# Kernel tuning notes

Hardware: AMD Instinct MI355X
Metric: run time of the kernel (lower is better)

## Reference

```python
import jax, jax.numpy as jnp
import numpy as np

B, N, D, H = 4, 2048, 256, 8
DH = D // H

def setup_inputs() -> dict:
    key = jax.random.key(0)
    ks = jax.random.split(key, 7)
    s = 1.0 / np.sqrt(DH)
    return {
        "sequences": jax.random.normal(ks[0], (B, N, D), dtype=jnp.float32),
        "Wq": jax.random.uniform(ks[1], (H, DH, DH), jnp.float32, -s, s),
        "bq": jax.random.uniform(ks[2], (H, DH), jnp.float32, -s, s),
        "Wk": jax.random.uniform(ks[3], (H, DH, DH), jnp.float32, -s, s),
        "bk": jax.random.uniform(ks[4], (H, DH), jnp.float32, -s, s),
        "Wv": jax.random.uniform(ks[5], (H, DH, DH), jnp.float32, -s, s),
        "bv": jax.random.uniform(ks[6], (H, DH), jnp.float32, -s, s),
    }

def reference(sequences, Wq, bq, Wk, bk, Wv, bv):
    # sequences: [B, N, D] -> [B, N, H, DH] (head h sees columns h*DH:(h+1)*DH)
    x = sequences.reshape(B, N, H, DH)
    # per-head Linear: y = x @ W.T + b
    q = jnp.einsum("bnhd,hed->bnhe", x, Wq) + bq
    k = jnp.einsum("bnhd,hed->bnhe", x, Wk) + bk
    v = jnp.einsum("bnhd,hed->bnhe", x, Wv) + bv
    scores = jnp.einsum("bnhe,bmhe->bhnm", q, k) / jnp.sqrt(jnp.float32(DH))
    attn = jax.nn.softmax(scores, axis=-1)  # [B, H, N, N]
    out = jnp.einsum("bhnm,bmhe->bnhe", attn, v)
    # hstack of per-head results == concat over last dim == reshape
    return out.reshape(B, N, D)
```

## Files before the change

### kernel.cpp

```cpp
#include <hip/hip_runtime.h>
#include <hip/hip_bf16.h>

typedef __bf16 bf16;
typedef __bf16 bf16x8 __attribute__((ext_vector_type(8)));
typedef __bf16 bf16x4 __attribute__((ext_vector_type(4)));
typedef float  f32x4  __attribute__((ext_vector_type(4)));

#define B_  4
#define N_  2048
#define D_  256
#define H_  8
#define DH_ 32
#define QKV_ELEMS (B_*H_*N_*DH_)

#define QSC    (0.17677669529663687f * 1.4426950408889634f)
#define NBIAS  (-17.312340490667562f)

#if __has_builtin(__builtin_amdgcn_exp2f)
__device__ inline float exp2_hw(float x) { return __builtin_amdgcn_exp2f(x); }
#else
__device__ inline float exp2_hw(float x) {
    float r; asm volatile("v_exp_f32 %0, %1" : "=v"(r) : "v"(x)); return r;
}
#endif

__device__ inline void gload_lds16(const bf16* g, bf16* l) {
    __builtin_amdgcn_global_load_lds(
        (const __attribute__((address_space(1))) void*)g,
        (__attribute__((address_space(3))) void*)l, 16, 0, 0);
}

__device__ inline bf16x8 ldcvt8(const float* __restrict__ p) {
    f32x4 a = *(const f32x4*)p;
    f32x4 b = *(const f32x4*)(p + 4);
    bf16x8 r;
    r[0] = (bf16)a[0]; r[1] = (bf16)a[1]; r[2] = (bf16)a[2]; r[3] = (bf16)a[3];
    r[4] = (bf16)b[0]; r[5] = (bf16)b[1]; r[6] = (bf16)b[2]; r[7] = (bf16)b[3];
    return r;
}

__global__ __launch_bounds__(256, 4) void qkv_proj_kernel(
    const float* __restrict__ x,
    const float* __restrict__ Wq, const float* __restrict__ bq,
    const float* __restrict__ Wk, const float* __restrict__ bk,
    const float* __restrict__ Wv, const float* __restrict__ bv,
    bf16* __restrict__ Qg, bf16* __restrict__ Kg, bf16* __restrict__ Vg)
{
    const int bh = blockIdx.x & 31, nt = blockIdx.x >> 5;
    const int h  = bh & (H_-1),    b  = bh >> 3;
    const int wave = threadIdx.x >> 6, lane = threadIdx.x & 63;
    const int l16 = lane & 15, q4 = lane >> 4;
    const int n0 = nt*64 + wave*16;

    bf16x8 wqf[2], wkf[2], wvf[2];
    f32x4  bq4[2], bk4[2];
    float  bvs[2];
    #pragma unroll
    for (int half = 0; half < 2; ++half) {
        wqf[half] = ldcvt8(Wq + (h*DH_ + half*16 + l16)*DH_ + q4*8);
        wkf[half] = ldcvt8(Wk + (h*DH_ + half*16 + l16)*DH_ + q4*8);
        wvf[half] = ldcvt8(Wv + (h*DH_ + half*16 + l16)*DH_ + q4*8);
        bq4[half] = *(const f32x4*)(bq + h*DH_ + half*16 + q4*4);
        bk4[half] = *(const f32x4*)(bk + h*DH_ + half*16 + q4*4);
        bvs[half] = bv[h*DH_ + half*16 + l16];
    }

    bf16x8 xf = ldcvt8(x + ((size_t)(b*N_ + n0 + l16))*D_ + h*DH_ + q4*8);
    const f32x4 z = {0.f,0.f,0.f,0.f};

    #pragma unroll
    for (int half = 0; half < 2; ++half) {
        f32x4 dq = __builtin_amdgcn_mfma_f32_16x16x32_bf16(wqf[half], xf, z, 0, 0, 0);
        f32x4 dk = __builtin_amdgcn_mfma_f32_16x16x32_bf16(wkf[half], xf, z, 0, 0, 0);
        f32x4 dv = __builtin_amdgcn_mfma_f32_16x16x32_bf16(xf, wvf[half], z, 0, 0, 0);
        bf16x4 pq, pk, pv;
        #pragma unroll
        for (int r = 0; r < 4; ++r) {
            pq[r] = (bf16)((dq[r] + bq4[half][r]) * QSC);
            pk[r] = (bf16)(dk[r] + bk4[half][r]);
            pv[r] = (bf16)(dv[r] + bvs[half]);
        }
        const size_t row = ((size_t)bh*N_ + n0 + l16)*DH_ + half*16 + q4*4;
        *(bf16x4*)(Qg + row) = pq;
        *(bf16x4*)(Kg + row) = pk;
        const int e = half*16 + l16;
        const size_t idx = ((size_t)bh << 16) + ((size_t)(n0 >> 5) << 10)
                         + (e << 5) + (q4 << 3) + (((n0 >> 4) & 1) << 2);
        *(bf16x4*)(Vg + idx) = pv;
    }
}

__global__ __launch_bounds__(256, 2) void attn_kernel(
    const bf16* __restrict__ Qg, const bf16* __restrict__ Kg,
    const bf16* __restrict__ Vg, float* __restrict__ out)
{
    const int bh = blockIdx.x & 31;
    const int qt = blockIdx.x >> 5;
    const int h  = bh & (H_-1), b = bh >> 3;
    const int lane = threadIdx.x & 63;
    const int wave = threadIdx.x >> 6;
    const int l16 = lane & 15, q4 = lane >> 4;

    __shared__ bf16 Kl[4][128*DH_];
    __shared__ bf16 Vl[4][128*DH_];

    const bf16* Kb = Kg + (size_t)bh*N_*DH_;
    const bf16* Vb = Vg + ((size_t)bh << 16);
    const int qrow0 = qt*128 + wave*32;
    const int kt0 = ((qt*5 + bh) & 7)*2;

    bf16x8 qb0 = *(const bf16x8*)(Qg + ((size_t)bh*N_ + qrow0 + l16)*DH_ + q4*8);
    bf16x8 qb1 = *(const bf16x8*)(Qg + ((size_t)bh*N_ + qrow0 + 16 + l16)*DH_ + q4*8);

    bf16x8 ones;
    #pragma unroll
    for (int j = 0; j < 8; ++j) ones[j] = (bf16)1.0f;

    f32x4 ot[2][2];
    ot[0][0] = (f32x4){0,0,0,0}; ot[0][1] = (f32x4){0,0,0,0};
    ot[1][0] = (f32x4){0,0,0,0}; ot[1][1] = (f32x4){0,0,0,0};
    f32x4 osum0 = {0,0,0,0}, osum1 = {0,0,0,0};
    const f32x4 zb = {NBIAS, NBIAS, NBIAS, NBIAS};

    const int seg = wave*1024 + lane*8;

    #pragma unroll
    for (int d = 0; d < 2; ++d) {
        const int t = (kt0 + d) & 15;
        const bf16* gk = Kb + (size_t)t*4096 + seg;
        const bf16* gv = Vb + (size_t)t*4096 + seg;
        gload_lds16(gk,       &Kl[d][wave*1024]);
        gload_lds16(gk + 512, &Kl[d][wave*1024 + 512]);
        gload_lds16(gv,       &Vl[d][wave*1024]);
        gload_lds16(gv + 512, &Vl[d][wave*1024 + 512]);
    }
    __syncthreads();

    for (int p = 0; p < 8; ++p) {
        #pragma unroll
        for (int d = 2; d < 4; ++d) {
            const int t  = (kt0 + 2*p + d) & 15;
            const int bf = (2*p + d) & 3;
            const bf16* gk = Kb + (size_t)t*4096 + seg;
            const bf16* gv = Vb + (size_t)t*4096 + seg;
            gload_lds16(gk,       &Kl[bf][wave*1024]);
            gload_lds16(gk + 512, &Kl[bf][wave*1024 + 512]);
            gload_lds16(gv,       &Vl[bf][wave*1024]);
            gload_lds16(gv + 512, &Vl[bf][wave*1024 + 512]);
        }

        #pragma unroll
        for (int d = 0; d < 2; ++d) {
            const int bf = (2*p + d) & 3;
            f32x4 st[8][2];
            #pragma unroll
            for (int kc = 0; kc < 8; ++kc) {
                bf16x8 kf = *(const bf16x8*)(&Kl[bf][(kc*16 + l16)*DH_ + q4*8]);
                st[kc][0] = __builtin_amdgcn_mfma_f32_16x16x32_bf16(kf, qb0, zb, 0, 0, 0);
                st[kc][1] = __builtin_amdgcn_mfma_f32_16x16x32_bf16(kf, qb1, zb, 0, 0, 0);
            }
            #pragma unroll
            for (int kk = 0; kk < 4; ++kk) {
                bf16x8 pb0, pb1;
                #pragma unroll
                for (int hf = 0; hf < 2; ++hf)
                    #pragma unroll
                    for (int r = 0; r < 4; ++r) {
                        pb0[hf*4 + r] = (bf16)exp2_hw(st[kk*2 + hf][0][r]);
                        pb1[hf*4 + r] = (bf16)exp2_hw(st[kk*2 + hf][1][r]);
                    }
                bf16x8 v0 = *(const bf16x8*)(&Vl[bf][kk*1024 + l16*DH_ + q4*8]);
                bf16x8 v1 = *(const bf16x8*)(&Vl[bf][kk*1024 + (16 + l16)*DH_ + q4*8]);
                ot[0][0] = __builtin_amdgcn_mfma_f32_16x16x32_bf16(v0, pb0, ot[0][0], 0, 0, 0);
                ot[1][0] = __builtin_amdgcn_mfma_f32_16x16x32_bf16(v1, pb0, ot[1][0], 0, 0, 0);
                ot[0][1] = __builtin_amdgcn_mfma_f32_16x16x32_bf16(v0, pb1, ot[0][1], 0, 0, 0);
                ot[1][1] = __builtin_amdgcn_mfma_f32_16x16x32_bf16(v1, pb1, ot[1][1], 0, 0, 0);
                osum0 = __builtin_amdgcn_mfma_f32_16x16x32_bf16(ones, pb0, osum0, 0, 0, 0);
                osum1 = __builtin_amdgcn_mfma_f32_16x16x32_bf16(ones, pb1, osum1, 0, 0, 0);
            }
        }

        __syncthreads();
    }

    const float inv0 = 1.0f / osum0[0], inv1 = 1.0f / osum1[0];

    #pragma unroll
    for (int qh = 0; qh < 2; ++qh) {
        const float inv = qh ? inv1 : inv0;
        #pragma unroll
        for (int dhh = 0; dhh < 2; ++dhh) {
            f32x4 w;
            #pragma unroll
            for (int r = 0; r < 4; ++r) w[r] = ot[dhh][qh][r] * inv;
            *(f32x4*)(out + ((size_t)b*N_ + qrow0 + qh*16 + l16)*D_
                          + h*DH_ + dhh*16 + q4*4) = w;
        }
    }
}

extern "C" void kernel_launch(void* const* d_in, const int* in_sizes, int n_in,
                              void* d_out, int out_size, void* d_ws, size_t ws_size,
                              hipStream_t stream)
{
    const float* x  = (const float*)d_in[0];
    const float* Wq = (const float*)d_in[1];
    const float* bq = (const float*)d_in[2];
    const float* Wk = (const float*)d_in[3];
    const float* bk = (const float*)d_in[4];
    const float* Wv = (const float*)d_in[5];
    const float* bv = (const float*)d_in[6];
    float* out = (float*)d_out;

    bf16* Qg = (bf16*)d_ws;
    bf16* Kg = Qg + QKV_ELEMS;
    bf16* Vg = Kg + QKV_ELEMS;

    qkv_proj_kernel<<<dim3(B_*H_*32), dim3(256), 0, stream>>>(
        x, Wq, bq, Wk, bk, Wv, bv, Qg, Kg, Vg);
    attn_kernel<<<dim3(B_*H_*(N_/128)), dim3(256), 0, stream>>>(Qg, Kg, Vg, out);
}
```

Measured before the change: 103.0 us.

## Give each wave private double-buffered K/V tiles and drop block barriers

The attention kernel previously shared 128-key K/V tiles across the block through a 4-deep LDS ring and synchronized with __syncthreads. Now each wave streams its own 64-key tiles into a private double buffer, waiting with s_waitcnt on vmcnt instead of block barriers, and each wave starts at a staggered tile. This removes block-wide barrier stalls and lets waves proceed independently. In exchange each wave loads K/V separately, which quadruples global/L2 traffic per block, and the pipeline is now only one tile deep.

```diff
diff --git a/kernel.cpp b/kernel.cpp
--- a/kernel.cpp
+++ b/kernel.cpp
@@ -29,6 +29,8 @@
         (const __attribute__((address_space(1))) void*)g,
         (__attribute__((address_space(3))) void*)l, 16, 0, 0);
 }
+
+#define WAITCNT_VM8 0x0F78
 
 __device__ inline bf16x8 ldcvt8(const float* __restrict__ p) {
     f32x4 a = *(const f32x4*)p;
@@ -101,13 +103,11 @@
     const int wave = threadIdx.x >> 6;
     const int l16 = lane & 15, q4 = lane >> 4;
 
-    __shared__ bf16 Kl[4][128*DH_];
-    __shared__ bf16 Vl[4][128*DH_];
+    __shared__ bf16 L[4][2][4096];
 
     const bf16* Kb = Kg + (size_t)bh*N_*DH_;
     const bf16* Vb = Vg + ((size_t)bh << 16);
     const int qrow0 = qt*128 + wave*32;
-    const int kt0 = ((qt*5 + bh) & 7)*2;
 
     bf16x8 qb0 = *(const bf16x8*)(Qg + ((size_t)bh*N_ + qrow0 + l16)*DH_ + q4*8);
     bf16x8 qb1 = *(const bf16x8*)(Qg + ((size_t)bh*N_ + qrow0 + 16 + l16)*DH_ + q4*8);
@@ -122,65 +122,64 @@
     f32x4 osum0 = {0,0,0,0}, osum1 = {0,0,0,0};
     const f32x4 zb = {NBIAS, NBIAS, NBIAS, NBIAS};
 
-    const int seg = wave*1024 + lane*8;
-
-    #pragma unroll
-    for (int d = 0; d < 2; ++d) {
-        const int t = (kt0 + d) & 15;
-        const bf16* gk = Kb + (size_t)t*4096 + seg;
-        const bf16* gv = Vb + (size_t)t*4096 + seg;
-        gload_lds16(gk,       &Kl[d][wave*1024]);
-        gload_lds16(gk + 512, &Kl[d][wave*1024 + 512]);
-        gload_lds16(gv,       &Vl[d][wave*1024]);
-        gload_lds16(gv + 512, &Vl[d][wave*1024 + 512]);
-    }
-    __syncthreads();
-
-    for (int p = 0; p < 8; ++p) {
-        #pragma unroll
-        for (int d = 2; d < 4; ++d) {
-            const int t  = (kt0 + 2*p + d) & 15;
-            const int bf = (2*p + d) & 3;
-            const bf16* gk = Kb + (size_t)t*4096 + seg;
-            const bf16* gv = Vb + (size_t)t*4096 + seg;
-            gload_lds16(gk,       &Kl[bf][wave*1024]);
-            gload_lds16(gk + 512, &Kl[bf][wave*1024 + 512]);
-            gload_lds16(gv,       &Vl[bf][wave*1024]);
-            gload_lds16(gv + 512, &Vl[bf][wave*1024 + 512]);
-        }
-
-        #pragma unroll
-        for (int d = 0; d < 2; ++d) {
-            const int bf = (2*p + d) & 3;
-            f32x4 st[8][2];
+    const int start = ((qt*5 + bh)*4 + wave) & 31;
+
+    {
+        const bf16* gk = Kb + (size_t)start*2048;
+        const bf16* gv = Vb + (size_t)start*2048;
+        #pragma unroll
+        for (int j = 0; j < 4; ++j) {
+            gload_lds16(gk + j*512 + lane*8, &L[wave][0][j*512]);
+            gload_lds16(gv + j*512 + lane*8, &L[wave][0][2048 + j*512]);
+        }
+    }
+
+    for (int i = 0; i < 32; ++i) {
+        const int cur = i & 1, nxt = cur ^ 1;
+        const int tn = (start + i + 1) & 31;
+
+        {
+            const bf16* gk = Kb + (size_t)tn*2048;
+            const bf16* gv = Vb + (size_t)tn*2048;
             #pragma unroll
-            for (int kc = 0; kc < 8; ++kc) {
-                bf16x8 kf = *(const bf16x8*)(&Kl[bf][(kc*16 + l16)*DH_ + q4*8]);
-                st[kc][0] = __builtin_amdgcn_mfma_f32_16x16x32_bf16(kf, qb0, zb, 0, 0, 0);
-                st[kc][1] = __builtin_amdgcn_mfma_f32_16x16x32_bf16(kf, qb1, zb, 0, 0, 0);
+            for (int j = 0; j < 4; ++j) {
+                gload_lds16(gk + j*512 + lane*8, &L[wave][nxt][j*512]);
+                gload_lds16(gv + j*512 + lane*8, &L[wave][nxt][2048 + j*512]);
             }
+        }
+
+        __builtin_amdgcn_s_waitcnt(WAITCNT_VM8);
+
+        const bf16* Kc = &L[wave][cur][0];
+        const bf16* Vc = &L[wave][cur][2048];
+
+        f32x4 st[4][2];
+        #pragma unroll
+        for (int kc = 0; kc < 4; ++kc) {
+            bf16x8 kf = *(const bf16x8*)(Kc + (kc*16 + l16)*DH_ + q4*8);
+            st[kc][0] = __builtin_amdgcn_mfma_f32_16x16x32_bf16(kf, qb0, zb, 0, 0, 0);
+            st[kc][1] = __builtin_amdgcn_mfma_f32_16x16x32_bf16(kf, qb1, zb, 0, 0, 0);
+        }
+
+        #pragma unroll
+        for (int kk = 0; kk < 2; ++kk) {
+            bf16x8 pb0, pb1;
             #pragma unroll
-            for (int kk = 0; kk < 4; ++kk) {
-                bf16x8 pb0, pb1;
+            for (int hf = 0; hf < 2; ++hf)
                 #pragma unroll
-                for (int hf = 0; hf < 2; ++hf)
-                    #pragma unroll
-                    for (int r = 0; r < 4; ++r) {
-                        pb0[hf*4 + r] = (bf16)exp2_hw(st[kk*2 + hf][0][r]);
-                        pb1[hf*4 + r] = (bf16)exp2_hw(st[kk*2 + hf][1][r]);
-                    }
-                bf16x8 v0 = *(const bf16x8*)(&Vl[bf][kk*1024 + l16*DH_ + q4*8]);
-                bf16x8 v1 = *(const bf16x8*)(&Vl[bf][kk*1024 + (16 + l16)*DH_ + q4*8]);
-                ot[0][0] = __builtin_amdgcn_mfma_f32_16x16x32_bf16(v0, pb0, ot[0][0], 0, 0, 0);
-                ot[1][0] = __builtin_amdgcn_mfma_f32_16x16x32_bf16(v1, pb0, ot[1][0], 0, 0, 0);
-                ot[0][1] = __builtin_amdgcn_mfma_f32_16x16x32_bf16(v0, pb1, ot[0][1], 0, 0, 0);
-                ot[1][1] = __builtin_amdgcn_mfma_f32_16x16x32_bf16(v1, pb1, ot[1][1], 0, 0, 0);
-                osum0 = __builtin_amdgcn_mfma_f32_16x16x32_bf16(ones, pb0, osum0, 0, 0, 0);
-                osum1 = __builtin_amdgcn_mfma_f32_16x16x32_bf16(ones, pb1, osum1, 0, 0, 0);
-            }
-        }
-
-        __syncthreads();
+                for (int r = 0; r < 4; ++r) {
+                    pb0[hf*4 + r] = (bf16)exp2_hw(st[kk*2 + hf][0][r]);
+                    pb1[hf*4 + r] = (bf16)exp2_hw(st[kk*2 + hf][1][r]);
+                }
+            bf16x8 v0 = *(const bf16x8*)(Vc + kk*1024 + l16*DH_ + q4*8);
+            bf16x8 v1 = *(const bf16x8*)(Vc + kk*1024 + (16 + l16)*DH_ + q4*8);
+            ot[0][0] = __builtin_amdgcn_mfma_f32_16x16x32_bf16(v0, pb0, ot[0][0], 0, 0, 0);
+            ot[1][0] = __builtin_amdgcn_mfma_f32_16x16x32_bf16(v1, pb0, ot[1][0], 0, 0, 0);
+            ot[0][1] = __builtin_amdgcn_mfma_f32_16x16x32_bf16(v0, pb1, ot[0][1], 0, 0, 0);
+            ot[1][1] = __builtin_amdgcn_mfma_f32_16x16x32_bf16(v1, pb1, ot[1][1], 0, 0, 0);
+            osum0 = __builtin_amdgcn_mfma_f32_16x16x32_bf16(ones, pb0, osum0, 0, 0, 0);
+            osum1 = __builtin_amdgcn_mfma_f32_16x16x32_bf16(ones, pb1, osum1, 0, 0, 0);
+        }
     }
 
     const float inv0 = 1.0f / osum0[0], inv1 = 1.0f / osum1[0];
```

New measurement: 105.0 us. Within noise of the previous version (+1.9%).
